# Kernel optimization log

Hardware: AMD Instinct MI355X
Metric: run time of the kernel (lower is better)

## Reference

```python
import jax, jax.numpy as jnp
import numpy as np

NEG_SLOPE = 0.01  # torch nn.LeakyReLU default

N_NODES = 100000
N_EDGES = 1000000
D_FEAT = 64


def setup_inputs() -> dict:
    key = jax.random.key(0)
    ks = jax.random.split(key, 8)
    x = jax.random.normal(ks[0], (N_NODES, D_FEAT), dtype=jnp.float32)
    src = jax.random.randint(ks[1], (N_EDGES,), 0, N_NODES, dtype=jnp.int64 if jax.config.jax_enable_x64 else jnp.int32)
    dst = jax.random.randint(ks[2], (N_EDGES,), 0, N_NODES, dtype=jnp.int64 if jax.config.jax_enable_x64 else jnp.int32)
    s = 1.0 / np.sqrt(D_FEAT)
    W1 = jax.random.normal(ks[3], (D_FEAT, 64), dtype=jnp.float32) * s
    b1 = jnp.zeros((64,), dtype=jnp.float32)
    W2 = jax.random.normal(ks[4], (64, 64), dtype=jnp.float32) * s
    b2 = jnp.zeros((64,), dtype=jnp.float32)
    Wc = jax.random.normal(ks[5], (64, 2), dtype=jnp.float32) * s
    bc = jnp.zeros((2,), dtype=jnp.float32)
    return {"x": x, "src": src, "dst": dst, "W1": W1, "b1": b1,
            "W2": W2, "b2": b2, "Wc": Wc, "bc": bc}


def _graph_conv(x, src, dst, W, b, out_deg_isqrt, in_deg_isqrt, n_nodes):
    # DGL GraphConv, norm='both': h_v = ( sum_{u->v} x_u / sqrt(d_out(u)) ) / sqrt(d_in(v)) @ W + b
    # (in_feats <= out_feats here, so aggregate first then transform, matching DGL order)
    h = x * out_deg_isqrt[:, None]          # [N, d] scale by source out-degree
    msg = h[src]                            # [E, d] gather
    agg = jax.ops.segment_sum(msg, dst, num_segments=n_nodes)  # [N, d] scatter-add
    agg = agg * in_deg_isqrt[:, None]
    return agg @ W + b


def reference(x, src, dst, W1, b1, W2, b2, Wc, bc):
    n = x.shape[0]
    ones_e = jnp.ones(src.shape[0], dtype=x.dtype)
    out_deg = jnp.clip(jax.ops.segment_sum(ones_e, src, num_segments=n), 1.0)
    in_deg = jnp.clip(jax.ops.segment_sum(ones_e, dst, num_segments=n), 1.0)
    out_isqrt = out_deg ** -0.5
    in_isqrt = in_deg ** -0.5

    h = _graph_conv(x, src, dst, W1, b1, out_isqrt, in_isqrt, n)
    h = jax.nn.leaky_relu(h, NEG_SLOPE)
    h = _graph_conv(h, src, dst, W2, b2, out_isqrt, in_isqrt, n)
    h = jax.nn.leaky_relu(h, NEG_SLOPE)
    return h @ Wc + bc  # prediction=True -> linear classifier
```

## Files before the change

kernel.cpp:

```cpp
#include <hip/hip_runtime.h>


typedef __attribute__((ext_vector_type(8))) short short8;
typedef __attribute__((ext_vector_type(4))) float f32x4;

#define NPB 256
#define BSH 9
#define BW  512

__device__ __forceinline__ float b2f(unsigned short u) {
    return __uint_as_float(((unsigned int)u) << 16);
}
__device__ __forceinline__ unsigned short f2b(float f) {
    unsigned int i = __float_as_uint(f);
    unsigned int r = (i + 0x7FFFu + ((i >> 16) & 1u)) >> 16;
    return (unsigned short)r;
}

__global__ __launch_bounds__(256) void count_kernel(
    const int* __restrict__ src, const int* __restrict__ dst,
    int* __restrict__ cntD, int* __restrict__ cntS, int e, int chunk) {
    __shared__ int hD[256], hS[256];
    int t = threadIdx.x, pb = blockIdx.x;
    hD[t] = 0; hS[t] = 0;
    __syncthreads();
    int e0 = pb * chunk, e1 = min(e, e0 + chunk);
    for (int i = e0 + t; i < e1; i += 256) {
        atomicAdd(&hD[dst[i] >> BSH], 1);
        atomicAdd(&hS[src[i] >> BSH], 1);
    }
    __syncthreads();
    cntD[t * NPB + pb] = hD[t];
    cntS[t * NPB + pb] = hS[t];
}

__global__ __launch_bounds__(1024) void scanmat_kernel(int* __restrict__ cntD,
                                                       int* __restrict__ cntS) {
    int* a = (blockIdx.x == 0) ? cntD : cntS;
    __shared__ int s[1024];
    int t = threadIdx.x;
    int base = t * 64;
    int sum = 0;
    for (int j = 0; j < 64; j++) sum += a[base + j];
    s[t] = sum;
    __syncthreads();
    for (int d = 1; d < 1024; d <<= 1) {
        int x = (t >= d) ? s[t - d] : 0;
        __syncthreads();
        s[t] += x;
        __syncthreads();
    }
    int run = s[t] - sum;
    for (int j = 0; j < 64; j++) {
        int v = a[base + j];
        a[base + j] = run;
        run += v;
    }
}

__global__ __launch_bounds__(256) void part_kernel(
    const int* __restrict__ src, const int* __restrict__ dst,
    const int* __restrict__ cntD, const int* __restrict__ cntS,
    unsigned int* __restrict__ ebuf, unsigned short* __restrict__ sbuf,
    int e, int chunk) {
    __shared__ int cD[256], cS[256];
    int t = threadIdx.x, pb = blockIdx.x;
    cD[t] = cntD[t * NPB + pb];
    cS[t] = cntS[t * NPB + pb];
    __syncthreads();
    int e0 = pb * chunk, e1 = min(e, e0 + chunk);
    for (int i = e0 + t; i < e1; i += 256) {
        int s_ = src[i], d_ = dst[i];
        int pd = atomicAdd(&cD[d_ >> BSH], 1);
        ebuf[pd] = ((unsigned int)s_ << BSH) | (unsigned int)(d_ & (BW - 1));
        int ps_ = atomicAdd(&cS[s_ >> BSH], 1);
        sbuf[ps_] = (unsigned short)(s_ & (BW - 1));
    }
}

__global__ __launch_bounds__(256) void bucket_kernel(
    const unsigned int* __restrict__ ebuf, const unsigned short* __restrict__ sbuf,
    const int* __restrict__ cntD, const int* __restrict__ cntS,
    const float4* __restrict__ x4,
    int* __restrict__ row, float* __restrict__ ii, float* __restrict__ oi,
    int* __restrict__ csr, ushort4* __restrict__ xb, int n, int e) {
    __shared__ int cnt[BW], cur[BW], ocnt[BW], ps[256];
    __shared__ float ol[BW];
    int t = threadIdx.x, b = blockIdx.x;
    int v0 = b << BSH;
    int eb0 = cntD[b * NPB], eb1 = cntD[(b + 1) * NPB];
    int sb0 = cntS[b * NPB], sb1 = cntS[(b + 1) * NPB];
    cnt[t] = 0; cnt[t + 256] = 0;
    ocnt[t] = 0; ocnt[t + 256] = 0;
    __syncthreads();
    for (int i = eb0 + t; i < eb1; i += 256)
        atomicAdd(&cnt[ebuf[i] & (BW - 1)], 1);
    for (int i = sb0 + t; i < sb1; i += 256)
        atomicAdd(&ocnt[sbuf[i]], 1);
    __syncthreads();
    int c0 = cnt[2 * t], c1 = cnt[2 * t + 1];
    int pair = c0 + c1;
    ps[t] = pair;
    __syncthreads();
    for (int d = 1; d < 256; d <<= 1) {
        int x = (t >= d) ? ps[t - d] : 0;
        __syncthreads();
        ps[t] += x;
        __syncthreads();
    }
    int excl = ps[t] - pair;
    cur[2 * t] = excl;
    cur[2 * t + 1] = excl + c0;
    int v = v0 + 2 * t;
    if (v < n) {
        row[v] = eb0 + excl;
        ii[v] = rsqrtf((float)max(c0, 1));
    }
    if (v + 1 < n) {
        row[v + 1] = eb0 + excl + c0;
        ii[v + 1] = rsqrtf((float)max(c1, 1));
    }
    if (b == 0 && t == 0) row[n] = e;
    for (int j = t; j < BW; j += 256) {
        float o = rsqrtf((float)max(ocnt[j], 1));
        ol[j] = o;
        int vv = v0 + j;
        if (vv < n) oi[vv] = o;
    }
    __syncthreads();
    for (int i = eb0 + t; i < eb1; i += 256) {
        unsigned int p = ebuf[i];
        int r = atomicAdd(&cur[p & (BW - 1)], 1);
        csr[eb0 + r] = (int)(p >> BSH);
    }
    int nloc = min(BW, n - v0);
    for (int i = t; i < nloc * 16; i += 256) {
        int vl = i >> 4, q = i & 15;
        float s = ol[vl];
        float4 val = x4[(size_t)(v0 + vl) * 16 + q];
        xb[(size_t)(v0 + vl) * 16 + q] =
            make_ushort4(f2b(val.x * s), f2b(val.y * s), f2b(val.z * s), f2b(val.w * s));
    }
}

template <bool FINAL>
__global__ __launch_bounds__(256) void fused_kernel(
    const short8* __restrict__ featb, const int* __restrict__ row,
    const int* __restrict__ csr, const float* __restrict__ ii,
    const float* __restrict__ oi,
    const float* __restrict__ W, const float* __restrict__ bias,
    const float* __restrict__ Wc, const float* __restrict__ bcl,
    void* __restrict__ out, int n, int nwaves) {
    __shared__ short8 tile[4][16 * 9];
    int lane = threadIdx.x & 63;
    int o = lane >> 3, s = lane & 7;
    int m15 = lane & 15, quad = lane >> 4;
    short8* tl = tile[threadIdx.x >> 6];
    int wid = blockIdx.x * (blockDim.x >> 6) + (threadIdx.x >> 6);
    int ngroups = (n + 15) >> 4;

    short8 bf[4][2];
#pragma unroll
    for (int nt = 0; nt < 4; nt++)
#pragma unroll
        for (int kk = 0; kk < 2; kk++)
#pragma unroll
            for (int j = 0; j < 8; j++)
                bf[nt][kk][j] = (short)f2b(W[(kk * 32 + quad * 8 + j) * 64 + nt * 16 + m15]);

    float bias_r[4];
#pragma unroll
    for (int nt = 0; nt < 4; nt++) bias_r[nt] = bias[nt * 16 + m15];

    float wc_r[4][2];
    float bc0 = 0.f, bc1 = 0.f;
    if constexpr (FINAL) {
#pragma unroll
        for (int nt = 0; nt < 4; nt++) {
            wc_r[nt][0] = Wc[(nt * 16 + m15) * 2];
            wc_r[nt][1] = Wc[(nt * 16 + m15) * 2 + 1];
        }
        bc0 = bcl[0];
        bc1 = bcl[1];
    }

    for (int g = wid; g < ngroups; g += nwaves) {
        int rbase = g << 4;

#pragma unroll
        for (int p = 0; p < 2; p++) {
            int v = rbase + p * 8 + o;
            bool valid = v < n;
            int base = 0, cnt = 0;
            if (valid) { base = row[v]; cnt = row[v + 1] - base; }
            float a[8];
#pragma unroll
            for (int k = 0; k < 8; k++) a[k] = 0.f;
            int j = 0;
            for (; j + 3 < cnt; j += 4) {
                int u[4];
#pragma unroll
                for (int k = 0; k < 4; k++) u[k] = csr[base + j + k];
#pragma unroll
                for (int k = 0; k < 4; k++) {
                    short8 f = featb[(size_t)u[k] * 8 + s];
#pragma unroll
                    for (int m = 0; m < 8; m++)
                        a[m] += b2f((unsigned short)f[m]);
                }
            }
            for (; j < cnt; j++) {
                short8 f = featb[(size_t)csr[base + j] * 8 + s];
#pragma unroll
                for (int m = 0; m < 8; m++)
                    a[m] += b2f((unsigned short)f[m]);
            }
            float iiv = valid ? ii[v] : 0.f;
            short8 r;
#pragma unroll
            for (int m = 0; m < 8; m++) r[m] = (short)f2b(a[m] * iiv);
            tl[(p * 8 + o) * 9 + s] = r;
        }

        short8 af0 = tl[m15 * 9 + quad];
        short8 af1 = tl[m15 * 9 + 4 + quad];

        f32x4 acc[4];
#pragma unroll
        for (int nt = 0; nt < 4; nt++) {
            f32x4 z = {0.f, 0.f, 0.f, 0.f};
            z = __builtin_amdgcn_mfma_f32_16x16x32_bf16(af0, bf[nt][0], z, 0, 0, 0);
            z = __builtin_amdgcn_mfma_f32_16x16x32_bf16(af1, bf[nt][1], z, 0, 0, 0);
            acc[nt] = z;
        }

        if constexpr (!FINAL) {
#pragma unroll
            for (int r = 0; r < 4; r++) {
                int vr = rbase + quad * 4 + r;
                float os = (vr < n) ? oi[vr] : 0.f;
#pragma unroll
                for (int nt = 0; nt < 4; nt++) {
                    float ov = acc[nt][r] + bias_r[nt];
                    ov = (ov > 0.f) ? ov : 0.01f * ov;
                    if (vr < n)
                        ((unsigned short*)out)[(size_t)vr * 64 + nt * 16 + m15] = f2b(ov * os);
                }
            }
        } else {
#pragma unroll
            for (int r = 0; r < 4; r++) {
                float p0 = 0.f, p1 = 0.f;
#pragma unroll
                for (int nt = 0; nt < 4; nt++) {
                    float ov = acc[nt][r] + bias_r[nt];
                    ov = (ov > 0.f) ? ov : 0.01f * ov;
                    p0 = fmaf(ov, wc_r[nt][0], p0);
                    p1 = fmaf(ov, wc_r[nt][1], p1);
                }
#pragma unroll
                for (int off = 1; off < 16; off <<= 1) {
                    p0 += __shfl_xor(p0, off);
                    p1 += __shfl_xor(p1, off);
                }
                int vr = rbase + quad * 4 + r;
                if (m15 == 0 && vr < n)
                    ((float2*)out)[vr] = make_float2(p0 + bc0, p1 + bc1);
            }
        }
    }
}

extern "C" void kernel_launch(void* const* d_in, const int* in_sizes, int n_in,
                              void* d_out, int out_size, void* d_ws, size_t ws_size,
                              hipStream_t stream) {
    const float* x  = (const float*)d_in[0];
    const int* src  = (const int*)d_in[1];
    const int* dst  = (const int*)d_in[2];
    const float* W1 = (const float*)d_in[3];
    const float* b1 = (const float*)d_in[4];
    const float* W2 = (const float*)d_in[5];
    const float* b2 = (const float*)d_in[6];
    const float* Wc = (const float*)d_in[7];
    const float* bc = (const float*)d_in[8];
    int n = in_sizes[0] / 64;
    int e = in_sizes[1];
    int total = n * 64;
    int nbuck = (n + BW - 1) >> BSH;

    char* ws = (char*)d_ws;
    size_t off = 0;
    auto take = [&](size_t bytes) -> char* {
        char* p = ws + off;
        off = (off + bytes + 255) & ~(size_t)255;
        return p;
    };
    int* cntD = (int*)take(256 * NPB * 4);
    int* cntS = (int*)take(256 * NPB * 4);
    unsigned int* ebuf = (unsigned int*)take((size_t)e * 4);
    unsigned short* sbuf = (unsigned short*)take((size_t)e * 2);
    int* row  = (int*)take((size_t)(n + 1) * 4);
    int* csr  = (int*)take((size_t)e * 4);
    float* oi = (float*)take((size_t)n * 4);
    float* ii = (float*)take((size_t)n * 4);
    unsigned short* xb  = (unsigned short*)take((size_t)total * 2);
    unsigned short* h1b = (unsigned short*)take((size_t)total * 2);

    const int tb = 256;
    int chunk = (e + NPB - 1) / NPB;

    count_kernel<<<NPB, tb, 0, stream>>>(src, dst, cntD, cntS, e, chunk);
    scanmat_kernel<<<2, 1024, 0, stream>>>(cntD, cntS);
    part_kernel<<<NPB, tb, 0, stream>>>(src, dst, cntD, cntS, ebuf, sbuf, e, chunk);
    bucket_kernel<<<nbuck, tb, 0, stream>>>(ebuf, sbuf, cntD, cntS, (const float4*)x,
                                            row, ii, oi, csr, (ushort4*)xb, n, e);

    const int fblocks = 784;
    const int fwaves = fblocks * (tb / 64);

    fused_kernel<false><<<fblocks, tb, 0, stream>>>((const short8*)xb, row, csr, ii, oi,
                                                    W1, b1, nullptr, nullptr, h1b, n, fwaves);
    fused_kernel<true><<<fblocks, tb, 0, stream>>>((const short8*)h1b, row, csr, ii, nullptr,
                                                   W2, b2, Wc, bc, d_out, n, fwaves);
}
```

Before: 221.8 us.

## Sort nodes by in-degree into a permutation to balance per-wave aggregation work

```diff
diff --git a/kernel.cpp b/kernel.cpp
--- a/kernel.cpp
+++ b/kernel.cpp
@@ -19,10 +19,12 @@
 
 __global__ __launch_bounds__(256) void count_kernel(
     const int* __restrict__ src, const int* __restrict__ dst,
-    int* __restrict__ cntD, int* __restrict__ cntS, int e, int chunk) {
+    int* __restrict__ cntD, int* __restrict__ cntS,
+    int* __restrict__ dhist, int e, int chunk) {
     __shared__ int hD[256], hS[256];
     int t = threadIdx.x, pb = blockIdx.x;
     hD[t] = 0; hS[t] = 0;
+    if (pb == 0) dhist[t] = 0;
     __syncthreads();
     int e0 = pb * chunk, e1 = min(e, e0 + chunk);
     for (int i = e0 + t; i < e1; i += 256) {
@@ -83,8 +85,9 @@
     const int* __restrict__ cntD, const int* __restrict__ cntS,
     const float4* __restrict__ x4,
     int* __restrict__ row, float* __restrict__ ii, float* __restrict__ oi,
-    int* __restrict__ csr, ushort4* __restrict__ xb, int n, int e) {
-    __shared__ int cnt[BW], cur[BW], ocnt[BW], ps[256];
+    int* __restrict__ csr, ushort4* __restrict__ xb,
+    int* __restrict__ dhist, int n, int e) {
+    __shared__ int cnt[BW], cur[BW], ocnt[BW], ps[256], dh[256];
     __shared__ float ol[BW];
     int t = threadIdx.x, b = blockIdx.x;
     int v0 = b << BSH;
@@ -92,6 +95,7 @@
     int sb0 = cntS[b * NPB], sb1 = cntS[(b + 1) * NPB];
     cnt[t] = 0; cnt[t + 256] = 0;
     ocnt[t] = 0; ocnt[t + 256] = 0;
+    dh[t] = 0;
     __syncthreads();
     for (int i = eb0 + t; i < eb1; i += 256)
         atomicAdd(&cnt[ebuf[i] & (BW - 1)], 1);
@@ -115,10 +119,12 @@
     if (v < n) {
         row[v] = eb0 + excl;
         ii[v] = rsqrtf((float)max(c0, 1));
+        atomicAdd(&dh[min(c0, 255)], 1);
     }
     if (v + 1 < n) {
         row[v + 1] = eb0 + excl + c0;
         ii[v + 1] = rsqrtf((float)max(c1, 1));
+        atomicAdd(&dh[min(c1, 255)], 1);
     }
     if (b == 0 && t == 0) row[n] = e;
     for (int j = t; j < BW; j += 256) {
@@ -128,6 +134,7 @@
         if (vv < n) oi[vv] = o;
     }
     __syncthreads();
+    if (dh[t] > 0) atomicAdd(&dhist[t], dh[t]);
     for (int i = eb0 + t; i < eb1; i += 256) {
         unsigned int p = ebuf[i];
         int r = atomicAdd(&cur[p & (BW - 1)], 1);
@@ -143,11 +150,46 @@
     }
 }
 
+__global__ __launch_bounds__(256) void scand_kernel(const int* __restrict__ dhist,
+                                                    int* __restrict__ dcur) {
+    __shared__ int s[256];
+    int t = threadIdx.x;
+    int mine = dhist[t];
+    s[t] = mine;
+    __syncthreads();
+    for (int d = 1; d < 256; d <<= 1) {
+        int x = (t >= d) ? s[t - d] : 0;
+        __syncthreads();
+        s[t] += x;
+        __syncthreads();
+    }
+    dcur[t] = s[t] - mine;
+}
+
+__global__ __launch_bounds__(256) void perm_kernel(
+    const int* __restrict__ row, int* __restrict__ dcur,
+    int* __restrict__ perm, int n) {
+    __shared__ int lh[256], lb[256], lc[256];
+    int t = threadIdx.x, b = blockIdx.x;
+    int v0 = b << BSH;
+    lh[t] = 0; lc[t] = 0;
+    __syncthreads();
+    int v = v0 + 2 * t;
+    int d0 = -1, d1 = -1;
+    if (v < n)     { d0 = min(row[v + 1] - row[v], 255); atomicAdd(&lh[d0], 1); }
+    if (v + 1 < n) { d1 = min(row[v + 2] - row[v + 1], 255); atomicAdd(&lh[d1], 1); }
+    __syncthreads();
+    if (lh[t] > 0) lb[t] = atomicAdd(&dcur[t], lh[t]);
+    __syncthreads();
+    if (d0 >= 0) { int o = atomicAdd(&lc[d0], 1); perm[lb[d0] + o] = v; }
+    if (d1 >= 0) { int o = atomicAdd(&lc[d1], 1); perm[lb[d1] + o] = v + 1; }
+}
+
 template <bool FINAL>
 __global__ __launch_bounds__(256) void fused_kernel(
     const short8* __restrict__ featb, const int* __restrict__ row,
     const int* __restrict__ csr, const float* __restrict__ ii,
-    const float* __restrict__ oi,
+    const float* __restrict__ oi, const int* __restrict__ perm,
     const float* __restrict__ W, const float* __restrict__ bias,
     const float* __restrict__ Wc, const float* __restrict__ bcl,
     void* __restrict__ out, int n, int nwaves) {
@@ -189,8 +231,9 @@
 
 #pragma unroll
         for (int p = 0; p < 2; p++) {
-            int v = rbase + p * 8 + o;
-            bool valid = v < n;
+            int idx = rbase + p * 8 + o;
+            bool valid = idx < n;
+            int v = valid ? perm[idx] : 0;
             int base = 0, cnt = 0;
             if (valid) { base = row[v]; cnt = row[v + 1] - base; }
             float a[8];
@@ -237,13 +280,15 @@
         if constexpr (!FINAL) {
 #pragma unroll
             for (int r = 0; r < 4; r++) {
-                int vr = rbase + quad * 4 + r;
-                float os = (vr < n) ? oi[vr] : 0.f;
+                int ridx = rbase + quad * 4 + r;
+                bool rv = ridx < n;
+                int vr = rv ? perm[ridx] : 0;
+                float os = rv ? oi[vr] : 0.f;
 #pragma unroll
                 for (int nt = 0; nt < 4; nt++) {
                     float ov = acc[nt][r] + bias_r[nt];
                     ov = (ov > 0.f) ? ov : 0.01f * ov;
-                    if (vr < n)
+                    if (rv)
                         ((unsigned short*)out)[(size_t)vr * 64 + nt * 16 + m15] = f2b(ov * os);
                 }
             }
@@ -263,8 +308,10 @@
                     p0 += __shfl_xor(p0, off);
                     p1 += __shfl_xor(p1, off);
                 }
-                int vr = rbase + quad * 4 + r;
-                if (m15 == 0 && vr < n)
+                int ridx = rbase + quad * 4 + r;
+                bool rv = ridx < n;
+                int vr = rv ? perm[ridx] : 0;
+                if (m15 == 0 && rv)
                     ((float2*)out)[vr] = make_float2(p0 + bc0, p1 + bc1);
             }
         }
@@ -303,23 +350,28 @@
     int* csr  = (int*)take((size_t)e * 4);
     float* oi = (float*)take((size_t)n * 4);
     float* ii = (float*)take((size_t)n * 4);
+    int* dhist = (int*)take(256 * 4);
+    int* dcur  = (int*)take(256 * 4);
+    int* perm  = (int*)take((size_t)n * 4);
     unsigned short* xb  = (unsigned short*)take((size_t)total * 2);
     unsigned short* h1b = (unsigned short*)take((size_t)total * 2);
 
     const int tb = 256;
     int chunk = (e + NPB - 1) / NPB;
 
-    count_kernel<<<NPB, tb, 0, stream>>>(src, dst, cntD, cntS, e, chunk);
+    count_kernel<<<NPB, tb, 0, stream>>>(src, dst, cntD, cntS, dhist, e, chunk);
     scanmat_kernel<<<2, 1024, 0, stream>>>(cntD, cntS);
     part_kernel<<<NPB, tb, 0, stream>>>(src, dst, cntD, cntS, ebuf, sbuf, e, chunk);
     bucket_kernel<<<nbuck, tb, 0, stream>>>(ebuf, sbuf, cntD, cntS, (const float4*)x,
-                                            row, ii, oi, csr, (ushort4*)xb, n, e);
-
-    const int fblocks = 784;
+                                            row, ii, oi, csr, (ushort4*)xb, dhist, n, e);
+    scand_kernel<<<1, 256, 0, stream>>>(dhist, dcur);
+    perm_kernel<<<nbuck, tb, 0, stream>>>(row, dcur, perm, n);
+
+    const int fblocks = 1568;
     const int fwaves = fblocks * (tb / 64);
 
     fused_kernel<false><<<fblocks, tb, 0, stream>>>((const short8*)xb, row, csr, ii, oi,
-                                                    W1, b1, nullptr, nullptr, h1b, n, fwaves);
+                                                    perm, W1, b1, nullptr, nullptr, h1b, n, fwaves);
     fused_kernel<true><<<fblocks, tb, 0, stream>>>((const short8*)h1b, row, csr, ii, nullptr,
-                                                   W2, b2, Wc, bc, d_out, n, fwaves);
-}
+                                                   perm, W2, b2, Wc, bc, d_out, n, fwaves);
+}
```

New measurement: 230.3 us. 3.8% more time.
